# Optimization experiments

Hardware: AMD Instinct MI355X
Metric: run time of the kernel (lower is better)

Reference implementation:

```python
import jax, jax.numpy as jnp
import numpy as np

TEMPERATURE = 0.07
EPS = 1e-8  # torch CosineSimilarity eps


def setup_inputs() -> dict:
    key = jax.random.key(0)
    k1, k2, k3 = jax.random.split(key, 3)
    N, D = 8192, 512
    features = jax.random.normal(k1, (N, D), dtype=jnp.float32)
    positive_mask = jax.random.randint(k2, (N, N), 0, 2, dtype=jnp.int32)
    negative_mask = jax.random.randint(k3, (N, N), 0, 2, dtype=jnp.int32)
    return {"features": features, "positive_mask": positive_mask, "negative_mask": negative_mask}


def reference(features, positive_mask, negative_mask):
    N = positive_mask.shape[0]
    self_contrast = 1.0 - jnp.eye(N, dtype=features.dtype)  # zero diagonal
    pos = positive_mask.astype(features.dtype) * self_contrast  # [N, N]
    neg = negative_mask.astype(features.dtype) * self_contrast  # [N, N]

    # cosine similarity via normalized matmul (same math as broadcasted CosineSimilarity)
    norm = jnp.maximum(jnp.linalg.norm(features, axis=1, keepdims=True), EPS)
    fn = features / norm  # [N, D]
    sim = jnp.matmul(fn, fn.T) / TEMPERATURE  # [N, N]

    logits_max = jax.lax.stop_gradient(jnp.max(sim, axis=1, keepdims=True))
    e = jnp.exp(sim - logits_max)  # [N, N]

    positives = e * pos
    log_neg_sum = jnp.log(jnp.sum(e * neg, axis=1, keepdims=True))  # [N, 1]
    log_prob = positives - log_neg_sum  # [N, N] (faithful to source: exp-masked, not log)

    cardinal = jnp.sum(pos, axis=1)
    cardinal = jnp.where(cardinal == 0, 1.0, cardinal)
    log_prob_sum = jnp.sum(log_prob * pos, axis=1)
    loss = -log_prob_sum / cardinal
    return jnp.mean(loss)
```

## Files before the change

### kernel.cpp

```cpp
#include <hip/hip_runtime.h>
#include <hip/hip_bf16.h>
#include <math.h>

#define NN 8192
#define DD 512
#define INV_T 14.285714285714286f

typedef __attribute__((ext_vector_type(8))) short s16x8;
typedef __attribute__((ext_vector_type(4))) float f32x4;

__device__ __forceinline__ unsigned short f32_to_bf16(float f) {
  unsigned int u = __float_as_uint(f);
  u += 0x7FFFu + ((u >> 16) & 1u);
  return (unsigned short)(u >> 16);
}

__device__ __forceinline__ void async16(const void* g, void* l) {
  __builtin_amdgcn_global_load_lds((__attribute__((address_space(1))) void*)(void*)g,
                                   (__attribute__((address_space(3))) void*)l,
                                   16, 0, 0);
}

__device__ __forceinline__ void consume_masks(const int* mv, int kdp, int t0,
                                              unsigned long long (*pk)[128][2],
                                              int lane) {
  #pragma unroll
  for (int j = 0; j < 16; ++j) {
    const unsigned long long b = __ballot(mv[j] != 0);
    if (lane == j) pk[kdp][t0 + (j >> 1)][j & 1] = b;
  }
}

__global__ __launch_bounds__(256) void normalize_kernel(const float* __restrict__ f,
                                                        unsigned short* __restrict__ fnb,
                                                        float* __restrict__ acc) {
  if (blockIdx.x < 96) acc[blockIdx.x * 256 + threadIdx.x] = 0.f;

  const int wave = threadIdx.x >> 6;
  const int lane = threadIdx.x & 63;
  const int row  = blockIdx.x * 4 + wave;
  const float* src = f + (size_t)row * DD + lane * 8;
  float4 v0 = *(const float4*)src;
  float4 v1 = *(const float4*)(src + 4);
  float ss = v0.x*v0.x + v0.y*v0.y + v0.z*v0.z + v0.w*v0.w
           + v1.x*v1.x + v1.y*v1.y + v1.z*v1.z + v1.w*v1.w;
  #pragma unroll
  for (int o = 32; o; o >>= 1) ss += __shfl_xor(ss, o);
  const float r = 1.0f / fmaxf(sqrtf(ss), 1e-8f);
  ushort4 a, b;
  a.x = f32_to_bf16(v0.x * r); a.y = f32_to_bf16(v0.y * r);
  a.z = f32_to_bf16(v0.z * r); a.w = f32_to_bf16(v0.w * r);
  b.x = f32_to_bf16(v1.x * r); b.y = f32_to_bf16(v1.y * r);
  b.z = f32_to_bf16(v1.z * r); b.w = f32_to_bf16(v1.w * r);
  unsigned short* dst = fnb + (size_t)row * DD + lane * 8;
  *(ushort4*)dst = a;
  *(ushort4*)(dst + 4) = b;
}

__global__ __launch_bounds__(256, 3) void fused_kernel(const unsigned short* __restrict__ fnb,
                                                       const int* __restrict__ posm,
                                                       const int* __restrict__ negm,
                                                       float* __restrict__ Spos,
                                                       float* __restrict__ Sneg,
                                                       float* __restrict__ Pcnt) {
  const int bid = blockIdx.x;
  int bi = (int)(64.5 - sqrt(64.5 * 64.5 - 2.0 * (double)bid));
  while (64 * bi - bi * (bi - 1) / 2 > bid) --bi;
  while (64 * (bi + 1) - (bi + 1) * bi / 2 <= bid) ++bi;
  const int bj = bi + (bid - (64 * bi - bi * (bi - 1) / 2));
  const int I = bi * 128;
  const int J = bj * 128;
  const bool offdiag = (bi != bj);

  const int tid  = threadIdx.x;
  const int wave = tid >> 6;
  const int lane = tid & 63;
  const int wm = wave >> 1;
  const int wn = wave & 1;
  const int q   = lane >> 4;
  const int c16 = lane & 15;

  __shared__ alignas(16) unsigned short lA[128 * 32];
  __shared__ alignas(16) unsigned short lB[128 * 32];
  __shared__ float sacc[2][128][3];
  __shared__ unsigned long long pk[4][128][2];
  for (int t = tid; t < 2 * 128 * 3; t += 256) ((float*)sacc)[t] = 0.f;

  f32x4 acc[4][4];
  const f32x4 z4 = {0.f, 0.f, 0.f, 0.f};
  #pragma unroll
  for (int mt = 0; mt < 4; ++mt)
    #pragma unroll
    for (int nt = 0; nt < 4; ++nt) acc[mt][nt] = z4;

  int mv[16];

  for (int kk = 0; kk < DD / 32; ++kk) {
    const int k0    = kk * 32;
    const int kd    = kk & 3;
    const int slice = kk >> 2;
    const bool mact = (kd < 2) || offdiag;

    if (kk > 0 && ((((kk - 1) & 3) < 2) || offdiag)) {
      consume_masks(mv, (kk - 1) & 3, ((kk - 1) >> 2) * 32 + wave * 8, pk, lane);
    }

    #pragma unroll
    for (int c = 0; c < 2; ++c) {
      const int fidx = tid + c * 256;
      const int L    = fidx >> 2;
      const int p    = fidx & 3;
      const int csrc = (p ^ ((L >> 1) & 3)) & 3;
      async16(fnb + (size_t)(I + L) * DD + k0 + csrc * 8, (char*)lA + fidx * 16);
      const int gB = 4 * (L & 31) + (L >> 5);
      async16(fnb + (size_t)(J + gB) * DD + k0 + csrc * 8, (char*)lB + fidx * 16);
    }
    __builtin_amdgcn_sched_barrier(0);

    if (mact) {
      const int rbase = (kd & 2) ? J : I;
      const int cbase = (kd & 2) ? I : J;
      const int* __restrict__ mp = (kd & 1) ? negm : posm;
      const int trow0 = slice * 32 + wave * 8;
      #pragma unroll
      for (int j = 0; j < 16; ++j) {
        const int trow = trow0 + (j >> 1);
        mv[j] = mp[(size_t)(rbase + trow) * NN + cbase + (j & 1) * 64 + lane];
      }
    }
    __builtin_amdgcn_sched_barrier(0);

    if (mact) asm volatile("s_waitcnt vmcnt(16)" ::: "memory");
    else      asm volatile("s_waitcnt vmcnt(0)"  ::: "memory");
    __builtin_amdgcn_sched_barrier(0);
    __builtin_amdgcn_s_barrier();
    __builtin_amdgcn_sched_barrier(0);

    s16x8 aF[4], bF[4];
    #pragma unroll
    for (int t = 0; t < 4; ++t) {
      const int arow = wm * 64 + t * 16 + c16;
      const int apos = (q ^ ((arow >> 1) & 3)) & 3;
      aF[t] = *(const s16x8*)((const char*)lA + arow * 64 + apos * 16);
      const int Lb = (wn * 16 + c16) | (t << 5);
      const int bpos = (q ^ ((Lb >> 1) & 3)) & 3;
      bF[t] = *(const s16x8*)((const char*)lB + Lb * 64 + bpos * 16);
    }
    #pragma unroll
    for (int mt = 0; mt < 4; ++mt)
      #pragma unroll
      for (int nt = 0; nt < 4; ++nt)
        acc[mt][nt] = __builtin_amdgcn_mfma_f32_16x16x32_bf16(aF[mt], bF[nt], acc[mt][nt], 0, 0, 0);

    __builtin_amdgcn_sched_barrier(0);
    __builtin_amdgcn_s_barrier();
    __builtin_amdgcn_sched_barrier(0);
  }

  if (offdiag) consume_masks(mv, 3, 3 * 32 + wave * 8, pk, lane);
  __syncthreads();

  #pragma unroll
  for (int mt = 0; mt < 4; ++mt)
    #pragma unroll
    for (int nt = 0; nt < 4; ++nt)
      #pragma unroll
      for (int r = 0; r < 4; ++r)
        acc[mt][nt][r] = __expf(acc[mt][nt][r] * INV_T - INV_T);

  const bool hasdiag = (bi == bj) && (wm == wn);
  const int cb = wn * 64 + 4 * c16;
  const int half = c16 >> 3;
  const int bsh  = 4 * (c16 & 7);

  #pragma unroll
  for (int mt = 0; mt < 4; ++mt) {
    const int rl = wm * 64 + mt * 16 + q * 4;
    #pragma unroll
    for (int r = 0; r < 4; ++r) {
      const int row = rl + r;
      const uint2 pw = *(const uint2*)&pk[0][row][wn];
      const uint2 nw = *(const uint2*)&pk[1][row][wn];
      const unsigned int p32 = half ? pw.y : pw.x;
      const unsigned int n32 = half ? nw.y : nw.x;
      float dsp = 0.f, dsn = 0.f, dpc = 0.f;
      #pragma unroll
      for (int nt = 0; nt < 4; ++nt) {
        float pf = (float)((p32 >> (bsh + nt)) & 1u);
        float nf = (float)((n32 >> (bsh + nt)) & 1u);
        if (hasdiag && (row == cb + nt)) { pf = 0.f; nf = 0.f; }
        const float e = acc[mt][nt][r];
        dsp = fmaf(e, pf, dsp);
        dsn = fmaf(e, nf, dsn);
        dpc += pf;
      }
      #pragma unroll
      for (int o = 1; o <= 8; o <<= 1) {
        dsp += __shfl_xor(dsp, o);
        dsn += __shfl_xor(dsn, o);
        dpc += __shfl_xor(dpc, o);
      }
      if (c16 == 0) {
        atomicAdd(&sacc[0][row][0], dsp);
        atomicAdd(&sacc[0][row][1], dsn);
        atomicAdd(&sacc[0][row][2], dpc);
      }
    }
  }

  if (offdiag) {
    #pragma unroll
    for (int nt = 0; nt < 4; ++nt) {
      const int trl = cb + nt;
      const uint2 pw = *(const uint2*)&pk[2][trl][wm];
      const uint2 nw = *(const uint2*)&pk[3][trl][wm];
      float ts = 0.f, tn = 0.f, tp = 0.f;
      #pragma unroll
      for (int mt = 0; mt < 4; ++mt) {
        const unsigned int p32 = (mt < 2) ? pw.x : pw.y;
        const unsigned int n32 = (mt < 2) ? nw.x : nw.y;
        #pragma unroll
        for (int r = 0; r < 4; ++r) {
          const int bit = (mt & 1) * 16 + q * 4 + r;
          const float pf = (float)((p32 >> bit) & 1u);
          const float nf = (float)((n32 >> bit) & 1u);
          const float e = acc[mt][nt][r];
          ts = fmaf(e, pf, ts);
          tn = fmaf(e, nf, tn);
          tp += pf;
        }
      }
      ts += __shfl_xor(ts, 16); ts += __shfl_xor(ts, 32);
      tn += __shfl_xor(tn, 16); tn += __shfl_xor(tn, 32);
      tp += __shfl_xor(tp, 16); tp += __shfl_xor(tp, 32);
      if (q == 0) {
        atomicAdd(&sacc[1][trl][0], ts);
        atomicAdd(&sacc[1][trl][1], tn);
        atomicAdd(&sacc[1][trl][2], tp);
      }
    }
  }

  __syncthreads();

  const int r = tid & 127;
  if (tid < 128) {
    atomicAdd(&Spos[I + r], sacc[0][r][0]);
    atomicAdd(&Sneg[I + r], sacc[0][r][1]);
    atomicAdd(&Pcnt[I + r], sacc[0][r][2]);
  } else if (offdiag) {
    atomicAdd(&Spos[J + r], sacc[1][r][0]);
    atomicAdd(&Sneg[J + r], sacc[1][r][1]);
    atomicAdd(&Pcnt[J + r], sacc[1][r][2]);
  }
}

__global__ __launch_bounds__(256) void finalize_kernel(const float* __restrict__ Spos,
                                                       const float* __restrict__ Sneg,
                                                       const float* __restrict__ Pcnt,
                                                       float* __restrict__ out) {
  float local = 0.f;
  for (int i = threadIdx.x; i < NN; i += 256) {
    const float sp = Spos[i], sn = Sneg[i], pc = Pcnt[i];
    const float card = (pc == 0.f) ? 1.f : pc;
    local += (logf(sn) * pc - sp) / card;
  }
  #pragma unroll
  for (int o = 32; o; o >>= 1) local += __shfl_xor(local, o);
  __shared__ float red[4];
  if ((threadIdx.x & 63) == 0) red[threadIdx.x >> 6] = local;
  __syncthreads();
  if (threadIdx.x == 0)
    out[0] = (red[0] + red[1] + red[2] + red[3]) * (1.0f / (float)NN);
}

extern "C" void kernel_launch(void* const* d_in, const int* in_sizes, int n_in,
                              void* d_out, int out_size, void* d_ws, size_t ws_size,
                              hipStream_t stream) {
  const float* feat = (const float*)d_in[0];
  const int* posm   = (const int*)d_in[1];
  const int* negm   = (const int*)d_in[2];
  float* out = (float*)d_out;

  char* ws = (char*)d_ws;
  unsigned short* fnb = (unsigned short*)ws;
  float* Spos = (float*)(ws + (size_t)8 * 1024 * 1024);
  float* Sneg = Spos + NN;
  float* Pcnt = Sneg + NN;

  normalize_kernel<<<NN / 4, 256, 0, stream>>>(feat, fnb, Spos);
  fused_kernel<<<2080, 256, 0, stream>>>(fnb, posm, negm, Spos, Sneg, Pcnt);
  finalize_kernel<<<1, 256, 0, stream>>>(Spos, Sneg, Pcnt, out);
}
```

Before: 589.3 us.

## Split fused kernel into MFMA compute waves and dedicated mask-loader waves

The block grows to 512 threads: four waves run the async feature loads and MFMA, and four new loader waves fetch the int mask tiles and pack them into bitmasks in LDS. Both groups stay in step through matched barriers. The goal is to keep the heavy mask streaming off the compute waves' instruction stream and vmcnt waits so mask traffic overlaps the GEMM. The pk array is padded to stride 3, likely to reduce LDS bank conflicts. In exchange the barrier pairing becomes fragile, and the larger block with launch bounds (512,4) may cap register use and occupancy.

Measured after the change: 583.6 us. No clear change (-1.0%).

```diff
diff --git a/kernel.cpp b/kernel.cpp
--- a/kernel.cpp
+++ b/kernel.cpp
@@ -22,7 +22,7 @@
 }
 
 __device__ __forceinline__ void consume_masks(const int* mv, int kdp, int t0,
-                                              unsigned long long (*pk)[128][2],
+                                              unsigned long long (*pk)[128][3],
                                               int lane) {
   #pragma unroll
   for (int j = 0; j < 16; ++j) {
@@ -57,7 +57,7 @@
   *(ushort4*)(dst + 4) = b;
 }
 
-__global__ __launch_bounds__(256, 3) void fused_kernel(const unsigned short* __restrict__ fnb,
+__global__ __launch_bounds__(512, 4) void fused_kernel(const unsigned short* __restrict__ fnb,
                                                        const int* __restrict__ posm,
                                                        const int* __restrict__ negm,
                                                        float* __restrict__ Spos,
@@ -75,168 +75,174 @@
   const int tid  = threadIdx.x;
   const int wave = tid >> 6;
   const int lane = tid & 63;
-  const int wm = wave >> 1;
-  const int wn = wave & 1;
+  const bool loader = wave >= 4;
+  const int gw  = wave & 3;
+  const int wm  = gw >> 1;
+  const int wn  = gw & 1;
   const int q   = lane >> 4;
   const int c16 = lane & 15;
 
   __shared__ alignas(16) unsigned short lA[128 * 32];
   __shared__ alignas(16) unsigned short lB[128 * 32];
   __shared__ float sacc[2][128][3];
-  __shared__ unsigned long long pk[4][128][2];
-  for (int t = tid; t < 2 * 128 * 3; t += 256) ((float*)sacc)[t] = 0.f;
+  __shared__ unsigned long long pk[4][128][3];
+  for (int t = tid; t < 2 * 128 * 3; t += 512) ((float*)sacc)[t] = 0.f;
 
   f32x4 acc[4][4];
-  const f32x4 z4 = {0.f, 0.f, 0.f, 0.f};
-  #pragma unroll
-  for (int mt = 0; mt < 4; ++mt)
-    #pragma unroll
-    for (int nt = 0; nt < 4; ++nt) acc[mt][nt] = z4;
-
   int mv[16];
 
-  for (int kk = 0; kk < DD / 32; ++kk) {
-    const int k0    = kk * 32;
-    const int kd    = kk & 3;
-    const int slice = kk >> 2;
-    const bool mact = (kd < 2) || offdiag;
-
-    if (kk > 0 && ((((kk - 1) & 3) < 2) || offdiag)) {
-      consume_masks(mv, (kk - 1) & 3, ((kk - 1) >> 2) * 32 + wave * 8, pk, lane);
-    }
-
-    #pragma unroll
-    for (int c = 0; c < 2; ++c) {
-      const int fidx = tid + c * 256;
-      const int L    = fidx >> 2;
-      const int p    = fidx & 3;
-      const int csrc = (p ^ ((L >> 1) & 3)) & 3;
-      async16(fnb + (size_t)(I + L) * DD + k0 + csrc * 8, (char*)lA + fidx * 16);
-      const int gB = 4 * (L & 31) + (L >> 5);
-      async16(fnb + (size_t)(J + gB) * DD + k0 + csrc * 8, (char*)lB + fidx * 16);
-    }
-    __builtin_amdgcn_sched_barrier(0);
-
-    if (mact) {
-      const int rbase = (kd & 2) ? J : I;
-      const int cbase = (kd & 2) ? I : J;
-      const int* __restrict__ mp = (kd & 1) ? negm : posm;
-      const int trow0 = slice * 32 + wave * 8;
-      #pragma unroll
-      for (int j = 0; j < 16; ++j) {
-        const int trow = trow0 + (j >> 1);
-        mv[j] = mp[(size_t)(rbase + trow) * NN + cbase + (j & 1) * 64 + lane];
-      }
-    }
-    __builtin_amdgcn_sched_barrier(0);
-
-    if (mact) asm volatile("s_waitcnt vmcnt(16)" ::: "memory");
-    else      asm volatile("s_waitcnt vmcnt(0)"  ::: "memory");
-    __builtin_amdgcn_sched_barrier(0);
-    __builtin_amdgcn_s_barrier();
-    __builtin_amdgcn_sched_barrier(0);
-
-    s16x8 aF[4], bF[4];
-    #pragma unroll
-    for (int t = 0; t < 4; ++t) {
-      const int arow = wm * 64 + t * 16 + c16;
-      const int apos = (q ^ ((arow >> 1) & 3)) & 3;
-      aF[t] = *(const s16x8*)((const char*)lA + arow * 64 + apos * 16);
-      const int Lb = (wn * 16 + c16) | (t << 5);
-      const int bpos = (q ^ ((Lb >> 1) & 3)) & 3;
-      bF[t] = *(const s16x8*)((const char*)lB + Lb * 64 + bpos * 16);
-    }
+  if (!loader) {
+    const f32x4 z4 = {0.f, 0.f, 0.f, 0.f};
     #pragma unroll
     for (int mt = 0; mt < 4; ++mt)
       #pragma unroll
+      for (int nt = 0; nt < 4; ++nt) acc[mt][nt] = z4;
+  }
+
+  for (int kk = 0; kk < DD / 32; ++kk) {
+    if (!loader) {
+      const int k0 = kk * 32;
+      #pragma unroll
+      for (int c = 0; c < 2; ++c) {
+        const int fidx = tid + c * 256;
+        const int L    = fidx >> 2;
+        const int p    = fidx & 3;
+        const int csrc = (p ^ ((L >> 1) & 3)) & 3;
+        async16(fnb + (size_t)(I + L) * DD + k0 + csrc * 8, (char*)lA + fidx * 16);
+        const int gB = 4 * (L & 31) + (L >> 5);
+        async16(fnb + (size_t)(J + gB) * DD + k0 + csrc * 8, (char*)lB + fidx * 16);
+      }
+      __syncthreads();
+
+      s16x8 aF[4], bF[4];
+      #pragma unroll
+      for (int t = 0; t < 4; ++t) {
+        const int arow = wm * 64 + t * 16 + c16;
+        const int apos = (q ^ ((arow >> 1) & 3)) & 3;
+        aF[t] = *(const s16x8*)((const char*)lA + arow * 64 + apos * 16);
+        const int Lb = (wn * 16 + c16) | (t << 5);
+        const int bpos = (q ^ ((Lb >> 1) & 3)) & 3;
+        bF[t] = *(const s16x8*)((const char*)lB + Lb * 64 + bpos * 16);
+      }
+      #pragma unroll
+      for (int mt = 0; mt < 4; ++mt)
+        #pragma unroll
+        for (int nt = 0; nt < 4; ++nt)
+          acc[mt][nt] = __builtin_amdgcn_mfma_f32_16x16x32_bf16(aF[mt], bF[nt], acc[mt][nt], 0, 0, 0);
+      __syncthreads();
+    } else {
+      const int lw = wave - 4;
+      if (kk > 0) {
+        const int pkd = (kk - 1) & 3;
+        if (pkd < 2 || offdiag) {
+          consume_masks(mv, pkd, ((kk - 1) >> 2) * 32 + lw * 8, pk, lane);
+        }
+      }
+      const int kd    = kk & 3;
+      const int slice = kk >> 2;
+      if (kd < 2 || offdiag) {
+        const int rbase = (kd & 2) ? J : I;
+        const int cbase = (kd & 2) ? I : J;
+        const int* __restrict__ mp = (kd & 1) ? negm : posm;
+        const int trow0 = slice * 32 + lw * 8;
+        #pragma unroll
+        for (int j = 0; j < 16; ++j) {
+          const int trow = trow0 + (j >> 1);
+          mv[j] = mp[(size_t)(rbase + trow) * NN + cbase + (j & 1) * 64 + lane];
+        }
+      }
+      __builtin_amdgcn_sched_barrier(0);
+      __builtin_amdgcn_s_barrier();
+      __builtin_amdgcn_sched_barrier(0);
+      __builtin_amdgcn_s_barrier();
+      __builtin_amdgcn_sched_barrier(0);
+    }
+  }
+
+  if (loader && offdiag) {
+    consume_masks(mv, 3, 3 * 32 + (wave - 4) * 8, pk, lane);
+  }
+  __syncthreads();
+
+  if (!loader) {
+    #pragma unroll
+    for (int mt = 0; mt < 4; ++mt)
+      #pragma unroll
       for (int nt = 0; nt < 4; ++nt)
-        acc[mt][nt] = __builtin_amdgcn_mfma_f32_16x16x32_bf16(aF[mt], bF[nt], acc[mt][nt], 0, 0, 0);
-
-    __builtin_amdgcn_sched_barrier(0);
-    __builtin_amdgcn_s_barrier();
-    __builtin_amdgcn_sched_barrier(0);
-  }
-
-  if (offdiag) consume_masks(mv, 3, 3 * 32 + wave * 8, pk, lane);
-  __syncthreads();
-
-  #pragma unroll
-  for (int mt = 0; mt < 4; ++mt)
+        #pragma unroll
+        for (int r = 0; r < 4; ++r)
+          acc[mt][nt][r] = __expf(acc[mt][nt][r] * INV_T - INV_T);
+
+    const bool hasdiag = (bi == bj) && (wm == wn);
+    const int cb = wn * 64 + 4 * c16;
+    const int half = c16 >> 3;
+    const int bsh  = 4 * (c16 & 7);
+
     #pragma unroll
-    for (int nt = 0; nt < 4; ++nt)
-      #pragma unroll
-      for (int r = 0; r < 4; ++r)
-        acc[mt][nt][r] = __expf(acc[mt][nt][r] * INV_T - INV_T);
-
-  const bool hasdiag = (bi == bj) && (wm == wn);
-  const int cb = wn * 64 + 4 * c16;
-  const int half = c16 >> 3;
-  const int bsh  = 4 * (c16 & 7);
-
-  #pragma unroll
-  for (int mt = 0; mt < 4; ++mt) {
-    const int rl = wm * 64 + mt * 16 + q * 4;
-    #pragma unroll
-    for (int r = 0; r < 4; ++r) {
-      const int row = rl + r;
-      const uint2 pw = *(const uint2*)&pk[0][row][wn];
-      const uint2 nw = *(const uint2*)&pk[1][row][wn];
-      const unsigned int p32 = half ? pw.y : pw.x;
-      const unsigned int n32 = half ? nw.y : nw.x;
-      float dsp = 0.f, dsn = 0.f, dpc = 0.f;
+    for (int mt = 0; mt < 4; ++mt) {
+      const int rl = wm * 64 + mt * 16 + q * 4;
+      #pragma unroll
+      for (int r = 0; r < 4; ++r) {
+        const int row = rl + r;
+        const uint2 pw = *(const uint2*)&pk[0][row][wn];
+        const uint2 nw = *(const uint2*)&pk[1][row][wn];
+        const unsigned int p32 = half ? pw.y : pw.x;
+        const unsigned int n32 = half ? nw.y : nw.x;
+        float dsp = 0.f, dsn = 0.f, dpc = 0.f;
+        #pragma unroll
+        for (int nt = 0; nt < 4; ++nt) {
+          float pf = (float)((p32 >> (bsh + nt)) & 1u);
+          float nf = (float)((n32 >> (bsh + nt)) & 1u);
+          if (hasdiag && (row == cb + nt)) { pf = 0.f; nf = 0.f; }
+          const float e = acc[mt][nt][r];
+          dsp = fmaf(e, pf, dsp);
+          dsn = fmaf(e, nf, dsn);
+          dpc += pf;
+        }
+        #pragma unroll
+        for (int o = 1; o <= 8; o <<= 1) {
+          dsp += __shfl_xor(dsp, o);
+          dsn += __shfl_xor(dsn, o);
+          dpc += __shfl_xor(dpc, o);
+        }
+        if (c16 == 0) {
+          atomicAdd(&sacc[0][row][0], dsp);
+          atomicAdd(&sacc[0][row][1], dsn);
+          atomicAdd(&sacc[0][row][2], dpc);
+        }
+      }
+    }
+
+    if (offdiag) {
       #pragma unroll
       for (int nt = 0; nt < 4; ++nt) {
-        float pf = (float)((p32 >> (bsh + nt)) & 1u);
-        float nf = (float)((n32 >> (bsh + nt)) & 1u);
-        if (hasdiag && (row == cb + nt)) { pf = 0.f; nf = 0.f; }
-        const float e = acc[mt][nt][r];
-        dsp = fmaf(e, pf, dsp);
-        dsn = fmaf(e, nf, dsn);
-        dpc += pf;
-      }
-      #pragma unroll
-      for (int o = 1; o <= 8; o <<= 1) {
-        dsp += __shfl_xor(dsp, o);
-        dsn += __shfl_xor(dsn, o);
-        dpc += __shfl_xor(dpc, o);
-      }
-      if (c16 == 0) {
-        atomicAdd(&sacc[0][row][0], dsp);
-        atomicAdd(&sacc[0][row][1], dsn);
-        atomicAdd(&sacc[0][row][2], dpc);
-      }
-    }
-  }
-
-  if (offdiag) {
-    #pragma unroll
-    for (int nt = 0; nt < 4; ++nt) {
-      const int trl = cb + nt;
-      const uint2 pw = *(const uint2*)&pk[2][trl][wm];
-      const uint2 nw = *(const uint2*)&pk[3][trl][wm];
-      float ts = 0.f, tn = 0.f, tp = 0.f;
-      #pragma unroll
-      for (int mt = 0; mt < 4; ++mt) {
-        const unsigned int p32 = (mt < 2) ? pw.x : pw.y;
-        const unsigned int n32 = (mt < 2) ? nw.x : nw.y;
-        #pragma unroll
-        for (int r = 0; r < 4; ++r) {
-          const int bit = (mt & 1) * 16 + q * 4 + r;
-          const float pf = (float)((p32 >> bit) & 1u);
-          const float nf = (float)((n32 >> bit) & 1u);
-          const float e = acc[mt][nt][r];
-          ts = fmaf(e, pf, ts);
-          tn = fmaf(e, nf, tn);
-          tp += pf;
-        }
-      }
-      ts += __shfl_xor(ts, 16); ts += __shfl_xor(ts, 32);
-      tn += __shfl_xor(tn, 16); tn += __shfl_xor(tn, 32);
-      tp += __shfl_xor(tp, 16); tp += __shfl_xor(tp, 32);
-      if (q == 0) {
-        atomicAdd(&sacc[1][trl][0], ts);
-        atomicAdd(&sacc[1][trl][1], tn);
-        atomicAdd(&sacc[1][trl][2], tp);
+        const int trl = cb + nt;
+        const uint2 pw = *(const uint2*)&pk[2][trl][wm];
+        const uint2 nw = *(const uint2*)&pk[3][trl][wm];
+        float ts = 0.f, tn = 0.f, tp = 0.f;
+        #pragma unroll
+        for (int mt = 0; mt < 4; ++mt) {
+          const unsigned int p32 = (mt < 2) ? pw.x : pw.y;
+          const unsigned int n32 = (mt < 2) ? nw.x : nw.y;
+          #pragma unroll
+          for (int r = 0; r < 4; ++r) {
+            const int bit = (mt & 1) * 16 + q * 4 + r;
+            const float pf = (float)((p32 >> bit) & 1u);
+            const float nf = (float)((n32 >> bit) & 1u);
+            const float e = acc[mt][nt][r];
+            ts = fmaf(e, pf, ts);
+            tn = fmaf(e, nf, tn);
+            tp += pf;
+          }
+        }
+        ts += __shfl_xor(ts, 16); ts += __shfl_xor(ts, 32);
+        tn += __shfl_xor(tn, 16); tn += __shfl_xor(tn, 32);
+        tp += __shfl_xor(tp, 16); tp += __shfl_xor(tp, 32);
+        if (q == 0) {
+          atomicAdd(&sacc[1][trl][0], ts);
+          atomicAdd(&sacc[1][trl][1], tn);
+          atomicAdd(&sacc[1][trl][2], tp);
+        }
       }
     }
   }
@@ -248,7 +254,7 @@
     atomicAdd(&Spos[I + r], sacc[0][r][0]);
     atomicAdd(&Sneg[I + r], sacc[0][r][1]);
     atomicAdd(&Pcnt[I + r], sacc[0][r][2]);
-  } else if (offdiag) {
+  } else if (tid < 256 && offdiag) {
     atomicAdd(&Spos[J + r], sacc[1][r][0]);
     atomicAdd(&Sneg[J + r], sacc[1][r][1]);
     atomicAdd(&Pcnt[J + r], sacc[1][r][2]);
@@ -289,6 +295,6 @@
   float* Pcnt = Sneg + NN;
 
   normalize_kernel<<<NN / 4, 256, 0, stream>>>(feat, fnb, Spos);
-  fused_kernel<<<2080, 256, 0, stream>>>(fnb, posm, negm, Spos, Sneg, Pcnt);
+  fused_kernel<<<2080, 512, 0, stream>>>(fnb, posm, negm, Spos, Sneg, Pcnt);
   finalize_kernel<<<1, 256, 0, stream>>>(Spos, Sneg, Pcnt, out);
 }
```
